# Performance work log

Hardware: AMD Instinct MI355X
Metric: run time of the kernel (lower is better)

Reference implementation:

```python
import jax, jax.numpy as jnp
import numpy as np

N_NODES = 10000
N_EDGES = 160000
IN_F = 128


def setup_inputs() -> dict:
    key = jax.random.key(0)
    ks = jax.random.split(key, 12)
    v = jax.random.normal(ks[0], (N_NODES, IN_F), dtype=jnp.float32)
    edge_index = jax.random.randint(ks[1], (2, N_EDGES), 0, N_NODES, dtype=jnp.int64)
    def w(k, K, fi, fo):
        # PyG Linear glorot init approx
        s = 1.0 / np.sqrt(fi)
        return jax.random.uniform(k, (K, fi, fo), jnp.float32, -s, s)
    W1 = w(ks[2], 3, IN_F, 128); b1 = jnp.zeros((128,), jnp.float32)
    W2 = w(ks[3], 3, 128, 256); b2 = jnp.zeros((256,), jnp.float32)
    W3 = w(ks[4], 3, 256, 512); b3 = jnp.zeros((512,), jnp.float32)
    Wmu = w(ks[5], 1, 512, 256)[0]; bmu = jnp.zeros((256,), jnp.float32)
    Wstd = w(ks[6], 1, 512, 256)[0]; bstd = jnp.zeros((256,), jnp.float32)
    return {"v": v, "edge_index": edge_index, "W1": W1, "b1": b1, "W2": W2,
            "b2": b2, "W3": W3, "b3": b3, "Wmu": Wmu, "bmu": bmu,
            "Wstd": Wstd, "bstd": bstd}


def _norm_weights(edge_index, n):
    # PyG get_laplacian('sym') with lambda_max=2.0 => L_hat = -D^{-1/2} A D^{-1/2}
    # (diagonal of scaled Laplacian becomes exactly 0, so self-loops are dropped)
    row, col = edge_index[0], edge_index[1]
    deg = jax.ops.segment_sum(jnp.ones((edge_index.shape[1],), jnp.float32), row,
                              num_segments=n)
    dis = jnp.where(deg > 0, 1.0 / jnp.sqrt(deg), 0.0)
    w = -dis[row] * dis[col]
    return row, col, w


def _cheb3(x, W, b, row, col, w, n):
    # Chebyshev recursion: Tx0=x, Tx1=L_hat x, Tx2=2 L_hat Tx1 - Tx0
    def prop(z):
        return jax.ops.segment_sum(w[:, None] * z[row], col, num_segments=n)
    tx0 = x
    tx1 = prop(tx0)
    tx2 = 2.0 * prop(tx1) - tx0
    return (jnp.einsum('ni,io->no', tx0, W[0])
            + jnp.einsum('ni,io->no', tx1, W[1])
            + jnp.einsum('ni,io->no', tx2, W[2]) + b)


def reference(v, edge_index, W1, b1, W2, b2, W3, b3, Wmu, bmu, Wstd, bstd):
    n = v.shape[0]
    row, col, w = _norm_weights(edge_index, n)
    x = jax.nn.relu(_cheb3(v, W1, b1, row, col, w, n))
    x = jax.nn.relu(_cheb3(x, W2, b2, row, col, w, n))
    x = jax.nn.relu(_cheb3(x, W3, b3, row, col, w, n))
    # K=1 ChebConv is a plain per-node linear (only Tx0 term)
    mu = x @ Wmu + bmu
    std = x @ Wstd + bstd
    return mu, std
```

## Files before the change

### kernel.cpp

```cpp
#include <hip/hip_runtime.h>
#include <hip/hip_bf16.h>


typedef __attribute__((ext_vector_type(8)))  short bf16x8;
typedef __attribute__((ext_vector_type(16))) float f32x16;
typedef unsigned short u16;

__device__ __forceinline__ u16 f2bf(float x) {
  union { float f; unsigned u; } c; c.f = x;
  return (u16)((c.u + 0x7fffu + ((c.u >> 16) & 1u)) >> 16);
}
__device__ __forceinline__ float bf2f(u16 u) {
  union { unsigned u; float f; } c; c.u = ((unsigned)u) << 16;
  return c.f;
}

__device__ __forceinline__ size_t apidx(int r, int k, int KSQ) {
  const int slot = (((r >> 6) * KSQ + (k >> 5)) << 2) + (((r >> 5) & 1) << 1) + ((k >> 4) & 1);
  return ((size_t)slot << 9) + (size_t)(((((k >> 3) & 1) << 5) | (r & 31)) << 3) + (k & 7);
}

__global__ void k_init(const unsigned* __restrict__ v, int nv, int* __restrict__ vflag,
                       const unsigned* __restrict__ ei, int ne, int* __restrict__ eflag,
                       float* __restrict__ deg, int* __restrict__ cnt, int n, int zb,
                       u16* __restrict__ outSent, int outN) {
  __shared__ unsigned red[256];
  if (blockIdx.x == 0) {
    int ok = 0;
    for (int i = threadIdx.x; i < nv; i += 256) {
      unsigned lo = v[i] & 0xffffu;
      unsigned ef = (lo >> 7) & 0xffu;
      if (ef >= 115u && ef <= 140u) ok++;
    }
    red[threadIdx.x] = (unsigned)ok;
    __syncthreads();
    for (int s = 128; s > 0; s >>= 1) {
      if (threadIdx.x < s) red[threadIdx.x] += red[threadIdx.x + s];
      __syncthreads();
    }
    if (threadIdx.x == 0) *vflag = ((int)red[0] < nv / 2) ? 1 : 0;
  } else if (blockIdx.x == 1) {
    unsigned acc = 0;
    for (int i = threadIdx.x; i < ne; i += 256)
      if (i & 1) acc |= ei[i];
    red[threadIdx.x] = acc;
    __syncthreads();
    for (int s = 128; s > 0; s >>= 1) {
      if (threadIdx.x < s) red[threadIdx.x] |= red[threadIdx.x + s];
      __syncthreads();
    }
    if (threadIdx.x == 0) *eflag = (red[0] == 0u) ? 1 : 0;
  } else if (blockIdx.x < 2 + zb) {
    int i = (blockIdx.x - 2) * 256 + threadIdx.x;
    if (i < n) { deg[i] = 0.0f; cnt[i] = 0; }
  } else {
    int i = (blockIdx.x - 2 - zb) * 256 + threadIdx.x;
    if (i < outN) outSent[i] = 0x3F00;
  }
}

__device__ __forceinline__ void wpack_dev(
    const void* __restrict__ W, int wflag, int K, int Fo,
    u16* __restrict__ dstHi, u16* __restrict__ dstLo, int blk, int tid) {
  const int t = blk * 256 + tid;
  const int KS = K >> 5;
  const int total = (Fo >> 6) * KS * 4;
  const int s = t >> 6;
  if (s >= total) return;
  const int lane = t & 63;
  const int fb = s & 3;
  const int sk = s >> 2;
  const int ks = sk % KS;
  const int nt = sk / KS;
  const int col = (nt << 6) + ((fb >> 1) << 5) + (lane & 31);
  const int row = (ks << 5) + ((fb & 1) << 4) + ((lane >> 5) << 3);
  bf16x8 hi;
  if (wflag) {
    const float* Wf = (const float*)W;
    bf16x8 lo;
#pragma unroll
    for (int j = 0; j < 8; j++) {
      float wv = Wf[(size_t)(row + j) * Fo + col];
      u16 h = f2bf(wv);
      hi[j] = (short)h;
      lo[j] = (short)f2bf(wv - bf2f(h));
    }
    *(bf16x8*)(dstLo + (size_t)s * 512 + lane * 8) = lo;
  } else {
    const u16* Wb = (const u16*)W;
#pragma unroll
    for (int j = 0; j < 8; j++)
      hi[j] = (short)Wb[(size_t)(row + j) * Fo + col];
  }
  *(bf16x8*)(dstHi + (size_t)s * 512 + lane * 8) = hi;
}

__global__ void k_pack(const void* __restrict__ W1, const void* __restrict__ W2,
                       const void* __restrict__ W3, const void* __restrict__ Wmu,
                       const void* __restrict__ Wstd,
                       u16* pW1h, u16* pW1l, u16* pW2h, u16* pW2l,
                       u16* pW3h, u16* pW3l, u16* pHh, u16* pHl,
                       const void* __restrict__ v, u16* __restrict__ xb,
                       u16* __restrict__ xh, int n4,
                       const int* __restrict__ flags,
                       int c1, int c2, int c3, int c4, int c5) {
  const int wflag = flags[1];
  const int b = blockIdx.x;
  const int tid = threadIdx.x;
  if (b < c1)      { wpack_dev(W1,   wflag, 384, 128, pW1h, pW1l, b,      tid); return; }
  if (b < c2)      { wpack_dev(W2,   wflag, 384, 256, pW2h, pW2l, b - c1, tid); return; }
  if (b < c3)      { wpack_dev(W3,   wflag, 768, 512, pW3h, pW3l, b - c2, tid); return; }
  if (b < c4)      { wpack_dev(Wmu,  wflag, 512, 256, pHh,           pHl,           b - c3, tid); return; }
  if (b < c5)      { wpack_dev(Wstd, wflag, 512, 256, pHh + 131072,  pHl + 131072,  b - c4, tid); return; }
  const int i = (b - c5) * 256 + tid;
  if (i >= n4) return;
  float val[4];
  if (wflag) {
    float4 t = ((const float4*)v)[i];
    val[0] = t.x; val[1] = t.y; val[2] = t.z; val[3] = t.w;
  } else {
    ushort4 t = ((const ushort4*)v)[i];
    val[0] = bf2f(t.x); val[1] = bf2f(t.y); val[2] = bf2f(t.z); val[3] = bf2f(t.w);
  }
  ushort4 ho;
  ho.x = f2bf(val[0]); ho.y = f2bf(val[1]);
  ho.z = f2bf(val[2]); ho.w = f2bf(val[3]);
  *(ushort4*)(xb + (size_t)i * 4) = ho;
  const int r  = i >> 5;
  const int k0 = (i & 31) << 2;
  const size_t pi = apidx(r, k0, 4);
  *(ushort4*)(xh + pi) = ho;
}


__global__ void k_decode(const void* __restrict__ ei, const int* __restrict__ eflag,
                         int E, int N, int* __restrict__ rowi, int* __restrict__ coli,
                         float* __restrict__ deg, int* __restrict__ cnt) {
  int e = blockIdx.x * blockDim.x + threadIdx.x;
  if (e >= E) return;
  int f = *eflag;
  int r, c;
  if (f) {
    const long long* q = (const long long*)ei;
    r = (int)q[e]; c = (int)q[e + E];
  } else {
    const int* q = (const int*)ei;
    r = q[e]; c = q[e + E];
  }
  r = min(max(r, 0), N - 1);
  c = min(max(c, 0), N - 1);
  rowi[e] = r; coli[e] = c;
  atomicAdd(&deg[r], 1.0f);
  atomicAdd(&cnt[c], 1);
}

__global__ __launch_bounds__(1024) void k_scan(const int* __restrict__ cnt,
                                               int* __restrict__ colPtr,
                                               int* __restrict__ cursor,
                                               const float* __restrict__ deg,
                                               float* __restrict__ dis, int n) {
  __shared__ int ws[16];
  const int t = threadIdx.x;
  const int lane = t & 63;
  const int w = t >> 6;
  int carry = 0;
  for (int base = 0; base < n; base += 1024) {
    int i = base + t;
    int v = (i < n) ? cnt[i] : 0;
    if (i < n) {
      float d = deg[i];
      dis[i] = (d > 0.f) ? rsqrtf(d) : 0.f;
    }
    int x = v;
#pragma unroll
    for (int off = 1; off < 64; off <<= 1) {
      int y = __shfl_up(x, off);
      if (lane >= off) x += y;
    }
    if (lane == 63) ws[w] = x;
    __syncthreads();
    if (w == 0) {
      int sv = (lane < 16) ? ws[lane] : 0;
#pragma unroll
      for (int off = 1; off < 16; off <<= 1) {
        int y = __shfl_up(sv, off);
        if (lane >= off) sv += y;
      }
      if (lane < 16) ws[lane] = sv;
    }
    __syncthreads();
    int woff = (w == 0) ? 0 : ws[w - 1];
    int incl = carry + woff + x;
    if (i < n) { colPtr[i + 1] = incl; cursor[i] = incl - v; }
    int tot = ws[15];
    __syncthreads();
    carry += tot;
  }
  if (t == 0) colPtr[0] = 0;
}

__global__ void k_place(const int* __restrict__ rowi, const int* __restrict__ coli,
                        const float* __restrict__ dis, int* __restrict__ cursor,
                        int2* __restrict__ edges, int E) {
  int e = blockIdx.x * blockDim.x + threadIdx.x;
  if (e >= E) return;
  int r = rowi[e], c = coli[e];
  float wv = -dis[r] * dis[c];
  int pos = atomicAdd(&cursor[c], 1);
  edges[pos] = make_int2(r, __float_as_int(wv));
}

__global__ __launch_bounds__(256) void k_prop128(
    const u16* __restrict__ z, const u16* __restrict__ base,
    u16* __restrict__ outB, u16* __restrict__ outH,
    const int* __restrict__ colPtr, const int2* __restrict__ edges,
    int N, float alpha, float beta) {
  const int lane = threadIdx.x & 63;
  const int c = blockIdx.x * 4 + (threadIdx.x >> 6);
  if (c >= N) return;
  const int half = lane >> 5;
  const int li = lane & 31;
  const int s = colPtr[c], e = colPtr[c + 1];
  float4 acc[4];
#pragma unroll
  for (int k = 0; k < 4; k++) acc[k] = make_float4(0.f, 0.f, 0.f, 0.f);

  for (int j0 = s; j0 < e; j0 += 64) {
    const int take = min(64, e - j0);
    int rI = 0; float wI = 0.f;
    if (j0 + lane < e) {
      int2 ew = edges[j0 + lane];
      rI = ew.x; wI = __int_as_float(ew.y);
    }
    for (int jj = 0; jj < take; jj += 32) {
      int rr[16]; float ww[16];
#pragma unroll
      for (int p = 0; p < 16; p++) {
        rr[p] = __shfl(rI, jj + 2 * p + half);
        ww[p] = __shfl(wI, jj + 2 * p + half);
      }
      ushort4 zz[16];
#pragma unroll
      for (int p = 0; p < 16; p++)
        zz[p] = *(const ushort4*)(z + (size_t)rr[p] * 128 + li * 4);
#pragma unroll
      for (int p = 0; p < 16; p++) {
        const float wk = ww[p];
        acc[p & 3].x = fmaf(wk, bf2f(zz[p].x), acc[p & 3].x);
        acc[p & 3].y = fmaf(wk, bf2f(zz[p].y), acc[p & 3].y);
        acc[p & 3].z = fmaf(wk, bf2f(zz[p].z), acc[p & 3].z);
        acc[p & 3].w = fmaf(wk, bf2f(zz[p].w), acc[p & 3].w);
      }
    }
  }

  float4 a;
  a.x = (acc[0].x + acc[1].x) + (acc[2].x + acc[3].x);
  a.y = (acc[0].y + acc[1].y) + (acc[2].y + acc[3].y);
  a.z = (acc[0].z + acc[1].z) + (acc[2].z + acc[3].z);
  a.w = (acc[0].w + acc[1].w) + (acc[2].w + acc[3].w);
  a.x += __shfl_xor(a.x, 32);
  a.y += __shfl_xor(a.y, 32);
  a.z += __shfl_xor(a.z, 32);
  a.w += __shfl_xor(a.w, 32);

  if (lane < 32) {
    float vv[4] = {alpha * a.x, alpha * a.y, alpha * a.z, alpha * a.w};
    const size_t o = (size_t)c * 128 + li * 4;
    if (base != nullptr) {
      ushort4 b = *(const ushort4*)(base + o);
      vv[0] = fmaf(beta, bf2f(b.x), vv[0]); vv[1] = fmaf(beta, bf2f(b.y), vv[1]);
      vv[2] = fmaf(beta, bf2f(b.z), vv[2]); vv[3] = fmaf(beta, bf2f(b.w), vv[3]);
    }
    ushort4 ho;
    ho.x = f2bf(vv[0]); ho.y = f2bf(vv[1]);
    ho.z = f2bf(vv[2]); ho.w = f2bf(vv[3]);
    if (outB) *(ushort4*)(outB + o) = ho;
    const size_t pi = apidx(c, li << 2, 4);
    *(ushort4*)(outH + pi) = ho;
  }
}

__global__ __launch_bounds__(256) void k_prop256(
    const u16* __restrict__ z, const u16* __restrict__ base,
    u16* __restrict__ outB, u16* __restrict__ outH,
    const int* __restrict__ colPtr, const int2* __restrict__ edges,
    int N, float alpha, float beta) {
  const int lane = threadIdx.x & 63;
  const int c = blockIdx.x * 4 + (threadIdx.x >> 6);
  if (c >= N) return;
  const int s = colPtr[c], e = colPtr[c + 1];
  float4 acc[4];
#pragma unroll
  for (int k = 0; k < 4; k++) acc[k] = make_float4(0.f, 0.f, 0.f, 0.f);

  for (int j0 = s; j0 < e; j0 += 64) {
    const int take = min(64, e - j0);
    int rI = 0; float wI = 0.f;
    if (j0 + lane < e) {
      int2 ew = edges[j0 + lane];
      rI = ew.x; wI = __int_as_float(ew.y);
    }
    for (int jj = 0; jj < take; jj += 16) {
      int rr[16]; float ww[16];
#pragma unroll
      for (int k = 0; k < 16; k++) {
        rr[k] = __shfl(rI, jj + k);
        ww[k] = __shfl(wI, jj + k);
      }
      ushort4 zz[16];
#pragma unroll
      for (int k = 0; k < 16; k++)
        zz[k] = *(const ushort4*)(z + (size_t)rr[k] * 256 + lane * 4);
#pragma unroll
      for (int k = 0; k < 16; k++) {
        const float wk = ww[k];
        acc[k & 3].x = fmaf(wk, bf2f(zz[k].x), acc[k & 3].x);
        acc[k & 3].y = fmaf(wk, bf2f(zz[k].y), acc[k & 3].y);
        acc[k & 3].z = fmaf(wk, bf2f(zz[k].z), acc[k & 3].z);
        acc[k & 3].w = fmaf(wk, bf2f(zz[k].w), acc[k & 3].w);
      }
    }
  }

  float vv[4] = {alpha * ((acc[0].x + acc[1].x) + (acc[2].x + acc[3].x)),
                 alpha * ((acc[0].y + acc[1].y) + (acc[2].y + acc[3].y)),
                 alpha * ((acc[0].z + acc[1].z) + (acc[2].z + acc[3].z)),
                 alpha * ((acc[0].w + acc[1].w) + (acc[2].w + acc[3].w))};
  const size_t o = (size_t)c * 256 + lane * 4;
  if (base != nullptr) {
    ushort4 b = *(const ushort4*)(base + o);
    vv[0] = fmaf(beta, bf2f(b.x), vv[0]); vv[1] = fmaf(beta, bf2f(b.y), vv[1]);
    vv[2] = fmaf(beta, bf2f(b.z), vv[2]); vv[3] = fmaf(beta, bf2f(b.w), vv[3]);
  }
  ushort4 ho;
  ho.x = f2bf(vv[0]); ho.y = f2bf(vv[1]);
  ho.z = f2bf(vv[2]); ho.w = f2bf(vv[3]);
  if (outB) *(ushort4*)(outB + o) = ho;
  const size_t pi = apidx(c, lane << 2, 8);
  *(ushort4*)(outH + pi) = ho;
}

__global__ __launch_bounds__(256, 4) void k_gemm_mfma(
    const u16* __restrict__ a0h, const u16* __restrict__ a0l,
    const u16* __restrict__ a1h, const u16* __restrict__ a1l,
    const u16* __restrict__ a2h, const u16* __restrict__ a2l,
    const u16* __restrict__ packHi, const u16* __restrict__ packLo,
    const void* __restrict__ bias, const void* __restrict__ bias2,
    const int* __restrict__ wflagp,
    int N, int Fi, int NQ, int Fo,
    u16* __restrict__ outB, u16* __restrict__ outH, u16* __restrict__ outL,
    u16* __restrict__ outB16, float* __restrict__ outB32, int relu, int headSplit) {
  const int wflag = *wflagp;
  const bool useLo = (a0l != nullptr);
  const int tid  = threadIdx.x;
  const int lane = tid & 63;
  const int w    = tid >> 6;
  const int wm   = w >> 1;
  const int wn   = w & 1;

  const int gx = gridDim.x;
  int wg = blockIdx.x + gx * blockIdx.y;
  {
    const int nwg = gx * gridDim.y;
    const int q = nwg >> 3, r = nwg & 7;
    const int xcd = wg & 7;
    const int idx = wg >> 3;
    wg = (xcd < r ? xcd * (q + 1) : r * (q + 1) + (xcd - r) * q) + idx;
  }
  const int nt = wg % gx;
  const int mt = wg / gx;
  const int n0 = nt << 6;
  const int m0 = mt << 6;
  const int KSQ   = Fi >> 5;
  const int qsh   = __builtin_ctz(KSQ);
  const int qmask = KSQ - 1;
  const int KS    = NQ << qsh;

  const int laneoff = lane << 3;

  f32x16 acc = {};

#pragma unroll 2
  for (int ks = 0; ks < KS; ks++) {
    const int q   = ks >> qsh;
    const int ksl = ks & qmask;
    const u16* Ah = (q == 0) ? a0h : (q == 1 ? a1h : a2h);
    const size_t abase = ((size_t)(mt * KSQ + ksl) << 2) * 512 + (size_t)((wm << 1) * 512) + laneoff;
    const bf16x8 aH0 = *(const bf16x8*)(Ah + abase);
    const bf16x8 aH1 = *(const bf16x8*)(Ah + abase + 512);
    const size_t bbase = (((size_t)(nt * KS + ks) << 2) + (wn << 1)) * 512 + laneoff;
    const bf16x8 b0 = *(const bf16x8*)(packHi + bbase);
    const bf16x8 b1 = *(const bf16x8*)(packHi + bbase + 512);

    acc = __builtin_amdgcn_mfma_f32_32x32x16_bf16(aH0, b0, acc, 0, 0, 0);
    acc = __builtin_amdgcn_mfma_f32_32x32x16_bf16(aH1, b1, acc, 0, 0, 0);
    if (useLo) {
      const u16* Al = (q == 0) ? a0l : (q == 1 ? a1l : a2l);
      const bf16x8 aL0 = *(const bf16x8*)(Al + abase);
      const bf16x8 aL1 = *(const bf16x8*)(Al + abase + 512);
      acc = __builtin_amdgcn_mfma_f32_32x32x16_bf16(aL0, b0, acc, 0, 0, 0);
      acc = __builtin_amdgcn_mfma_f32_32x32x16_bf16(aL1, b1, acc, 0, 0, 0);
    }
    if (wflag) {
      const bf16x8 c0 = *(const bf16x8*)(packLo + bbase);
      const bf16x8 c1 = *(const bf16x8*)(packLo + bbase + 512);
      acc = __builtin_amdgcn_mfma_f32_32x32x16_bf16(aH0, c0, acc, 0, 0, 0);
      acc = __builtin_amdgcn_mfma_f32_32x32x16_bf16(aH1, c1, acc, 0, 0, 0);
    }
  }

  {
    const int ncol = n0 + (wn << 5) + (lane & 31);
    const int KSQo = Fo >> 5;
    int col = ncol;
    const void* bp = bias;
    size_t obase = 0;
    int FoOut = Fo;
    if (headSplit) {
      FoOut = 256;
      if (ncol >= 256) { col = ncol - 256; bp = bias2; obase = (size_t)N * 256; }
    }
    const float bv = wflag ? ((const float*)bp)[col]
                           : bf2f(((const u16*)bp)[col]);
#pragma unroll
    for (int r = 0; r < 16; r++) {
      const int m = m0 + (wm << 5) + (r & 3) + ((r >> 2) << 3) + ((lane >> 5) << 2);
      if (m < N) {
        float vv = acc[r] + bv;
        if (relu) vv = fmaxf(vv, 0.f);
        if (outH) {
          u16 h = f2bf(vv);
          const size_t pi = apidx(m, ncol, KSQo);
          outH[pi] = h;
          if (outL) outL[pi] = f2bf(vv - bf2f(h));
          if (outB) outB[(size_t)m * Fo + ncol] = h;
        }
        if (outB16) {
          const size_t o = obase + (size_t)m * FoOut + col;
          if (wflag) outB32[o] = vv;
          else       outB16[o] = f2bf(vv);
        }
      }
    }
  }
}


static size_t align256(size_t x) { return (x + 255) & ~(size_t)255; }

extern "C" void kernel_launch(void* const* d_in, const int* in_sizes, int n_in,
                              void* d_out, int out_size, void* d_ws, size_t ws_size,
                              hipStream_t stream) {
  const void* v    = d_in[0];
  const void* ei   = d_in[1];
  const void* W1   = d_in[2];
  const void* b1   = d_in[3];
  const void* W2   = d_in[4];
  const void* b2   = d_in[5];
  const void* W3   = d_in[6];
  const void* b3   = d_in[7];
  const void* Wmu  = d_in[8];
  const void* bmu  = d_in[9];
  const void* Wstd = d_in[10];
  const void* bstd = d_in[11];
  (void)n_in; (void)ws_size;

  const int N = in_sizes[0] / 128;
  const int E = in_sizes[1] / 2;
  const size_t NP = ((size_t)N + 63) & ~(size_t)63;

  char* base = (char*)d_ws;
  size_t off = 0;
  auto carve = [&](size_t bytes) { void* p = base + off; off = align256(off + bytes); return p; };

  int*   eflag  = (int*)  carve(4);
  int*   vflag  = (int*)  carve(4);
  int*   rowi   = (int*)  carve((size_t)E * 4);
  int*   coli   = (int*)  carve((size_t)E * 4);
  float* deg    = (float*)carve((size_t)N * 4);
  float* dis    = (float*)carve((size_t)N * 4);
  int*   cnt    = (int*)  carve((size_t)N * 4);
  int*   colPtr = (int*)  carve((size_t)(N + 1) * 4);
  int*   cursor = (int*)  carve((size_t)N * 4);
  int2*  edges  = (int2*) carve((size_t)E * 8);

  u16* pW1h = (u16*)carve((size_t)384 * 128 * 2);
  u16* pW1l = (u16*)carve((size_t)384 * 128 * 2);
  u16* pW2h = (u16*)carve((size_t)384 * 256 * 2);
  u16* pW2l = (u16*)carve((size_t)384 * 256 * 2);
  u16* pW3h = (u16*)carve((size_t)768 * 512 * 2);
  u16* pW3l = (u16*)carve((size_t)768 * 512 * 2);
  u16* pHh  = (u16*)carve((size_t)2 * 512 * 256 * 2);
  u16* pHl  = (u16*)carve((size_t)2 * 512 * 256 * 2);

  u16* Xb  = (u16*)carve(NP * 256 * 2);
  u16* Xh  = (u16*)carve(NP * 256 * 2);
  u16* Yb  = (u16*)carve(NP * 128 * 2);
  u16* Yh  = (u16*)carve(NP * 512 * 2);
  u16* Yl  = (u16*)carve(NP * 512 * 2);
  u16* t1b = (u16*)carve(NP * 256 * 2);
  u16* t1h = (u16*)carve(NP * 256 * 2);
  u16* t2h = (u16*)carve(NP * 256 * 2);

  const int zb = (N + 255) / 256;
  const int sb = (out_size + 255) / 256;
  k_init<<<2 + zb + sb, 256, 0, stream>>>((const unsigned*)v, 1024, vflag,
                                          (const unsigned*)ei, 2048, eflag,
                                          deg, cnt, N, zb, (u16*)d_out, out_size);

  const int n4 = N * 128 / 4;
  const int c1 = 24, c2 = c1 + 48, c3 = c2 + 192, c4 = c3 + 64, c5 = c4 + 64;
  const int cTot = c5 + (n4 + 255) / 256;
  k_pack<<<cTot, 256, 0, stream>>>(W1, W2, W3, Wmu, Wstd,
                                   pW1h, pW1l, pW2h, pW2l, pW3h, pW3l, pHh, pHl,
                                   v, Xb, Xh, n4, eflag,
                                   c1, c2, c3, c4, c5);

  k_decode<<<(E + 255) / 256, 256, 0, stream>>>(ei, eflag, E, N, rowi, coli, deg, cnt);
  k_scan<<<1, 1024, 0, stream>>>(cnt, colPtr, cursor, deg, dis, N);
  k_place<<<(E + 255) / 256, 256, 0, stream>>>(rowi, coli, dis, cursor, edges, E);

  const int gM = (N + 63) / 64;
  const int gP = (N + 3) / 4;

  k_prop128<<<gP, 256, 0, stream>>>(Xb, nullptr, t1b, t1h, colPtr, edges, N, 1.f, 0.f);
  k_prop128<<<gP, 256, 0, stream>>>(t1b, Xb, nullptr, t2h, colPtr, edges, N, 2.f, -1.f);
  k_gemm_mfma<<<dim3(2, gM), 256, 0, stream>>>(Xh, nullptr, t1h, nullptr, t2h, nullptr,
                                               pW1h, pW1l, b1, b1, vflag, N, 128, 3, 128,
                                               Yb, Yh, nullptr, nullptr, nullptr, 1, 0);

  k_prop128<<<gP, 256, 0, stream>>>(Yb, nullptr, t1b, t1h, colPtr, edges, N, 1.f, 0.f);
  k_prop128<<<gP, 256, 0, stream>>>(t1b, Yb, nullptr, t2h, colPtr, edges, N, 2.f, -1.f);
  k_gemm_mfma<<<dim3(4, gM), 256, 0, stream>>>(Yh, nullptr, t1h, nullptr, t2h, nullptr,
                                               pW2h, pW2l, b2, b2, vflag, N, 128, 3, 256,
                                               Xb, Xh, nullptr, nullptr, nullptr, 1, 0);

  k_prop256<<<gP, 256, 0, stream>>>(Xb, nullptr, t1b, t1h, colPtr, edges, N, 1.f, 0.f);
  k_prop256<<<gP, 256, 0, stream>>>(t1b, Xb, nullptr, t2h, colPtr, edges, N, 2.f, -1.f);
  k_gemm_mfma<<<dim3(8, gM), 256, 0, stream>>>(Xh, nullptr, t1h, nullptr, t2h, nullptr,
                                               pW3h, pW3l, b3, b3, vflag, N, 256, 3, 512,
                                               nullptr, Yh, Yl, nullptr, nullptr, 1, 0);

  k_gemm_mfma<<<dim3(8, gM), 256, 0, stream>>>(Yh, Yl, nullptr, nullptr, nullptr, nullptr,
                                               pHh, pHl, bmu, bstd, vflag, N, 512, 1, 512,
                                               nullptr, nullptr, nullptr,
                                               (u16*)d_out, (float*)d_out, 0, 1);
}
```

Baseline: 292.0 us.

## Widen prop gathers to 16-byte loads and drop low-bf16 split for head GEMM

Both propagation kernels now gather neighbour rows with 8-element bf16 vector loads instead of 4-element ones. k_prop128 handles four edges per wavefront step (16 lanes per row), and k_prop256 handles two (32 lanes per row), with a shuffle reduction and half-wave or quarter-wave stores. This means fewer, wider memory transactions per gathered row and fewer in-flight loads per lane. Separately, the layer-3 GEMM no longer writes a low-order bf16 residual and the head GEMM reads only the high part. That removes a buffer write and read but reduces the precision of the mu/std head input.

```diff
diff --git a/kernel.cpp b/kernel.cpp
--- a/kernel.cpp
+++ b/kernel.cpp
@@ -218,12 +218,11 @@
   const int lane = threadIdx.x & 63;
   const int c = blockIdx.x * 4 + (threadIdx.x >> 6);
   if (c >= N) return;
-  const int half = lane >> 5;
-  const int li = lane & 31;
+  const int q4 = lane >> 4;
+  const int li = lane & 15;
   const int s = colPtr[c], e = colPtr[c + 1];
-  float4 acc[4];
-#pragma unroll
-  for (int k = 0; k < 4; k++) acc[k] = make_float4(0.f, 0.f, 0.f, 0.f);
+  float accA[8] = {0.f, 0.f, 0.f, 0.f, 0.f, 0.f, 0.f, 0.f};
+  float accB[8] = {0.f, 0.f, 0.f, 0.f, 0.f, 0.f, 0.f, 0.f};
 
   for (int j0 = s; j0 < e; j0 += 64) {
     const int take = min(64, e - j0);
@@ -232,52 +231,52 @@
       int2 ew = edges[j0 + lane];
       rI = ew.x; wI = __int_as_float(ew.y);
     }
-    for (int jj = 0; jj < take; jj += 32) {
-      int rr[16]; float ww[16];
-#pragma unroll
-      for (int p = 0; p < 16; p++) {
-        rr[p] = __shfl(rI, jj + 2 * p + half);
-        ww[p] = __shfl(wI, jj + 2 * p + half);
+    for (int pp = 0; pp < take; pp += 16) {
+      int rr[4]; float ww[4];
+#pragma unroll
+      for (int p = 0; p < 4; p++) {
+        rr[p] = __shfl(rI, pp + p * 4 + q4);
+        ww[p] = __shfl(wI, pp + p * 4 + q4);
       }
-      ushort4 zz[16];
-#pragma unroll
-      for (int p = 0; p < 16; p++)
-        zz[p] = *(const ushort4*)(z + (size_t)rr[p] * 128 + li * 4);
-#pragma unroll
-      for (int p = 0; p < 16; p++) {
+      bf16x8 zz[4];
+#pragma unroll
+      for (int p = 0; p < 4; p++)
+        zz[p] = *(const bf16x8*)(z + (size_t)rr[p] * 128 + li * 8);
+#pragma unroll
+      for (int p = 0; p < 4; p++) {
         const float wk = ww[p];
-        acc[p & 3].x = fmaf(wk, bf2f(zz[p].x), acc[p & 3].x);
-        acc[p & 3].y = fmaf(wk, bf2f(zz[p].y), acc[p & 3].y);
-        acc[p & 3].z = fmaf(wk, bf2f(zz[p].z), acc[p & 3].z);
-        acc[p & 3].w = fmaf(wk, bf2f(zz[p].w), acc[p & 3].w);
+        float* A = (p & 1) ? accB : accA;
+#pragma unroll
+        for (int j = 0; j < 8; j++)
+          A[j] = fmaf(wk, bf2f((u16)zz[p][j]), A[j]);
       }
     }
   }
 
-  float4 a;
-  a.x = (acc[0].x + acc[1].x) + (acc[2].x + acc[3].x);
-  a.y = (acc[0].y + acc[1].y) + (acc[2].y + acc[3].y);
-  a.z = (acc[0].z + acc[1].z) + (acc[2].z + acc[3].z);
-  a.w = (acc[0].w + acc[1].w) + (acc[2].w + acc[3].w);
-  a.x += __shfl_xor(a.x, 32);
-  a.y += __shfl_xor(a.y, 32);
-  a.z += __shfl_xor(a.z, 32);
-  a.w += __shfl_xor(a.w, 32);
-
-  if (lane < 32) {
-    float vv[4] = {alpha * a.x, alpha * a.y, alpha * a.z, alpha * a.w};
-    const size_t o = (size_t)c * 128 + li * 4;
+  float a[8];
+#pragma unroll
+  for (int j = 0; j < 8; j++) {
+    a[j] = accA[j] + accB[j];
+    a[j] += __shfl_xor(a[j], 16);
+    a[j] += __shfl_xor(a[j], 32);
+  }
+
+  if (lane < 16) {
+    const size_t o = (size_t)c * 128 + li * 8;
+    float vv[8];
+#pragma unroll
+    for (int j = 0; j < 8; j++) vv[j] = alpha * a[j];
     if (base != nullptr) {
-      ushort4 b = *(const ushort4*)(base + o);
-      vv[0] = fmaf(beta, bf2f(b.x), vv[0]); vv[1] = fmaf(beta, bf2f(b.y), vv[1]);
-      vv[2] = fmaf(beta, bf2f(b.z), vv[2]); vv[3] = fmaf(beta, bf2f(b.w), vv[3]);
-    }
-    ushort4 ho;
-    ho.x = f2bf(vv[0]); ho.y = f2bf(vv[1]);
-    ho.z = f2bf(vv[2]); ho.w = f2bf(vv[3]);
-    if (outB) *(ushort4*)(outB + o) = ho;
-    const size_t pi = apidx(c, li << 2, 4);
-    *(ushort4*)(outH + pi) = ho;
+      bf16x8 b = *(const bf16x8*)(base + o);
+#pragma unroll
+      for (int j = 0; j < 8; j++) vv[j] = fmaf(beta, bf2f((u16)b[j]), vv[j]);
+    }
+    bf16x8 ho;
+#pragma unroll
+    for (int j = 0; j < 8; j++) ho[j] = (short)f2bf(vv[j]);
+    if (outB) *(bf16x8*)(outB + o) = ho;
+    const size_t pi = apidx(c, li << 3, 4);
+    *(bf16x8*)(outH + pi) = ho;
   }
 }
 
@@ -289,10 +288,11 @@
   const int lane = threadIdx.x & 63;
   const int c = blockIdx.x * 4 + (threadIdx.x >> 6);
   if (c >= N) return;
+  const int h2 = lane >> 5;
+  const int li = lane & 31;
   const int s = colPtr[c], e = colPtr[c + 1];
-  float4 acc[4];
-#pragma unroll
-  for (int k = 0; k < 4; k++) acc[k] = make_float4(0.f, 0.f, 0.f, 0.f);
+  float accA[8] = {0.f, 0.f, 0.f, 0.f, 0.f, 0.f, 0.f, 0.f};
+  float accB[8] = {0.f, 0.f, 0.f, 0.f, 0.f, 0.f, 0.f, 0.f};
 
   for (int j0 = s; j0 < e; j0 += 64) {
     const int take = min(64, e - j0);
@@ -301,44 +301,52 @@
       int2 ew = edges[j0 + lane];
       rI = ew.x; wI = __int_as_float(ew.y);
     }
-    for (int jj = 0; jj < take; jj += 16) {
-      int rr[16]; float ww[16];
-#pragma unroll
-      for (int k = 0; k < 16; k++) {
-        rr[k] = __shfl(rI, jj + k);
-        ww[k] = __shfl(wI, jj + k);
+    for (int pp = 0; pp < take; pp += 8) {
+      int rr[4]; float ww[4];
+#pragma unroll
+      for (int p = 0; p < 4; p++) {
+        rr[p] = __shfl(rI, pp + p * 2 + h2);
+        ww[p] = __shfl(wI, pp + p * 2 + h2);
       }
-      ushort4 zz[16];
-#pragma unroll
-      for (int k = 0; k < 16; k++)
-        zz[k] = *(const ushort4*)(z + (size_t)rr[k] * 256 + lane * 4);
-#pragma unroll
-      for (int k = 0; k < 16; k++) {
-        const float wk = ww[k];
-        acc[k & 3].x = fmaf(wk, bf2f(zz[k].x), acc[k & 3].x);
-        acc[k & 3].y = fmaf(wk, bf2f(zz[k].y), acc[k & 3].y);
-        acc[k & 3].z = fmaf(wk, bf2f(zz[k].z), acc[k & 3].z);
-        acc[k & 3].w = fmaf(wk, bf2f(zz[k].w), acc[k & 3].w);
+      bf16x8 zz[4];
+#pragma unroll
+      for (int p = 0; p < 4; p++)
+        zz[p] = *(const bf16x8*)(z + (size_t)rr[p] * 256 + li * 8);
+#pragma unroll
+      for (int p = 0; p < 4; p++) {
+        const float wk = ww[p];
+        float* A = (p & 1) ? accB : accA;
+#pragma unroll
+        for (int j = 0; j < 8; j++)
+          A[j] = fmaf(wk, bf2f((u16)zz[p][j]), A[j]);
       }
     }
   }
 
-  float vv[4] = {alpha * ((acc[0].x + acc[1].x) + (acc[2].x + acc[3].x)),
-                 alpha * ((acc[0].y + acc[1].y) + (acc[2].y + acc[3].y)),
-                 alpha * ((acc[0].z + acc[1].z) + (acc[2].z + acc[3].z)),
-                 alpha * ((acc[0].w + acc[1].w) + (acc[2].w + acc[3].w))};
-  const size_t o = (size_t)c * 256 + lane * 4;
-  if (base != nullptr) {
-    ushort4 b = *(const ushort4*)(base + o);
-    vv[0] = fmaf(beta, bf2f(b.x), vv[0]); vv[1] = fmaf(beta, bf2f(b.y), vv[1]);
-    vv[2] = fmaf(beta, bf2f(b.z), vv[2]); vv[3] = fmaf(beta, bf2f(b.w), vv[3]);
-  }
-  ushort4 ho;
-  ho.x = f2bf(vv[0]); ho.y = f2bf(vv[1]);
-  ho.z = f2bf(vv[2]); ho.w = f2bf(vv[3]);
-  if (outB) *(ushort4*)(outB + o) = ho;
-  const size_t pi = apidx(c, lane << 2, 8);
-  *(ushort4*)(outH + pi) = ho;
+  float a[8];
+#pragma unroll
+  for (int j = 0; j < 8; j++) {
+    a[j] = accA[j] + accB[j];
+    a[j] += __shfl_xor(a[j], 32);
+  }
+
+  if (lane < 32) {
+    const size_t o = (size_t)c * 256 + li * 8;
+    float vv[8];
+#pragma unroll
+    for (int j = 0; j < 8; j++) vv[j] = alpha * a[j];
+    if (base != nullptr) {
+      bf16x8 b = *(const bf16x8*)(base + o);
+#pragma unroll
+      for (int j = 0; j < 8; j++) vv[j] = fmaf(beta, bf2f((u16)b[j]), vv[j]);
+    }
+    bf16x8 ho;
+#pragma unroll
+    for (int j = 0; j < 8; j++) ho[j] = (short)f2bf(vv[j]);
+    if (outB) *(bf16x8*)(outB + o) = ho;
+    const size_t pi = apidx(c, li << 3, 8);
+    *(bf16x8*)(outH + pi) = ho;
+  }
 }
 
 __global__ __launch_bounds__(256, 4) void k_gemm_mfma(
@@ -498,7 +506,6 @@
   u16* Xh  = (u16*)carve(NP * 256 * 2);
   u16* Yb  = (u16*)carve(NP * 128 * 2);
   u16* Yh  = (u16*)carve(NP * 512 * 2);
-  u16* Yl  = (u16*)carve(NP * 512 * 2);
   u16* t1b = (u16*)carve(NP * 256 * 2);
   u16* t1h = (u16*)carve(NP * 256 * 2);
   u16* t2h = (u16*)carve(NP * 256 * 2);
@@ -540,9 +547,9 @@
   k_prop256<<<gP, 256, 0, stream>>>(t1b, Xb, nullptr, t2h, colPtr, edges, N, 2.f, -1.f);
   k_gemm_mfma<<<dim3(8, gM), 256, 0, stream>>>(Xh, nullptr, t1h, nullptr, t2h, nullptr,
                                                pW3h, pW3l, b3, b3, vflag, N, 256, 3, 512,
-                                               nullptr, Yh, Yl, nullptr, nullptr, 1, 0);
-
-  k_gemm_mfma<<<dim3(8, gM), 256, 0, stream>>>(Yh, Yl, nullptr, nullptr, nullptr, nullptr,
+                                               nullptr, Yh, nullptr, nullptr, nullptr, 1, 0);
+
+  k_gemm_mfma<<<dim3(8, gM), 256, 0, stream>>>(Yh, nullptr, nullptr, nullptr, nullptr, nullptr,
                                                pHh, pHl, bmu, bstd, vflag, N, 512, 1, 512,
                                                nullptr, nullptr, nullptr,
                                                (u16*)d_out, (float*)d_out, 0, 1);
```

Result: faster. 272.1 us (-6.8%).
